# Optimization experiments

Measured on AMD Instinct MI355X. Metric: run time of the kernel, lower is better.

Reference implementation:

```python
import jax, jax.numpy as jnp
import numpy as np

N = 8192
IN_DIM = 256
OUT_DIM = 256


def setup_inputs() -> dict:
    key = jax.random.key(0)
    k1, k2, k3, k4 = jax.random.split(key, 4)
    x = jax.random.normal(k1, (N, IN_DIM), dtype=jnp.float32)
    adj = jax.random.uniform(k2, (N, N), dtype=jnp.float32)
    # nn.Linear(in_dim, out_dim): weight [out,in], bias [out]. Store W as [in,out].
    bound = 1.0 / np.sqrt(IN_DIM)
    W = jax.random.uniform(k3, (IN_DIM, OUT_DIM), dtype=jnp.float32, minval=-bound, maxval=bound)
    b = jax.random.uniform(k4, (OUT_DIM,), dtype=jnp.float32, minval=-bound, maxval=bound)
    return {"x": x, "adj": adj, "W": W, "b": b}


def reference(x, adj, W, b):
    # ReLU( D^{-1/2} (A + I) D^{-1/2} X W + b )
    # A_hat = adj + I; degree = A_hat.sum(axis=1)
    n = adj.shape[0]
    A_hat = adj + jnp.eye(n, dtype=adj.dtype)
    degree = A_hat.sum(axis=1)
    d_inv_sqrt = degree ** -0.5  # [N]
    # D^{-1/2} @ A_hat @ D^{-1/2} == row-scale then col-scale (no NxN diag matmuls)
    A_norm = A_hat * d_inv_sqrt[:, None] * d_inv_sqrt[None, :]
    out = A_norm @ x          # [N, in_dim]
    out = out @ W + b         # [N, out_dim]
    return jax.nn.relu(out)
```

## Files before the change

kernel.cpp:

```cpp
#include <hip/hip_runtime.h>


typedef __attribute__((ext_vector_type(8))) short short8;
typedef __attribute__((ext_vector_type(4))) float floatx4;

#define GLDS16(g, l) __builtin_amdgcn_global_load_lds(\
    (const __attribute__((address_space(1))) void*)(g), \
    (__attribute__((address_space(3))) void*)(l), 16, 0, 0)

__device__ __forceinline__ unsigned short f2b(float f) {
  unsigned int x = __builtin_bit_cast(unsigned int, f);
  unsigned int r = (x + 0x7fffu + ((x >> 16) & 1u)) >> 16;
  return (unsigned short)r;
}

__global__ __launch_bounds__(512) void k_deg(
    const float* __restrict__ adj, unsigned short* __restrict__ adjb,
    float* __restrict__ degree8) {
  __shared__ __align__(16) char xlds[65536];
  const int t = threadIdx.x, g = t >> 5, c = t & 31;
  const int mb2 = blockIdx.x >> 3, sk = (blockIdx.x >> 1) & 3, h = blockIdx.x & 1;
  const float* src = adj + (size_t)mb2 * 128 * 8192 + sk * 2048 + h * 1024;
  unsigned short* dstP = adjb
      + ((size_t)(mb2 * 4 + sk) * 32768 + (size_t)h * 16384) * 8;
  float rs[8] = {};
#pragma unroll
  for (int s = 0; s < 4; ++s) {
#pragma unroll
    for (int rr = 0; rr < 8; ++rr) {
      const int row = rr * 16 + g;
      const float* p = src + (size_t)row * 8192 + s * 256 + c * 8;
      float4 v0 = *(const float4*)(p);
      float4 v1 = *(const float4*)(p + 4);
      rs[rr] += ((v0.x + v0.y) + (v0.z + v0.w)) + ((v1.x + v1.y) + (v1.z + v1.w));
      short8 u;
      u[0] = f2b(v0.x); u[1] = f2b(v0.y); u[2] = f2b(v0.z); u[3] = f2b(v0.w);
      u[4] = f2b(v1.x); u[5] = f2b(v1.y); u[6] = f2b(v1.z); u[7] = f2b(v1.w);
      *(short8*)(xlds + c * 2048 + ((row ^ (c & 7)) * 16)) = u;
    }
    __syncthreads();
    unsigned short* dst = dstP + (size_t)s * 4096 * 8;
#pragma unroll
    for (int j = 0; j < 8; ++j) {
      const int lu = j * 512 + t;
      const int U = lu >> 7, R = lu & 127;
      short8 u = *(const short8*)(xlds + U * 2048 + ((R ^ (U & 7)) * 16));
      *(short8*)(dst + (size_t)lu * 8) = u;
    }
    __syncthreads();
  }
#pragma unroll
  for (int rr = 0; rr < 8; ++rr) {
#pragma unroll
    for (int o = 16; o > 0; o >>= 1) rs[rr] += __shfl_down(rs[rr], o, 32);
  }
  if (c == 0) {
    float* dp = degree8 + (size_t)(sk * 2 + h) * 8192 + mb2 * 128;
#pragma unroll
    for (int rr = 0; rr < 8; ++rr) dp[rr * 16 + g] = rs[rr];
  }
}

__global__ __launch_bounds__(256) void k_xw(
    const float* __restrict__ X, const float* __restrict__ W,
    const float* __restrict__ bias, const float* __restrict__ degree8,
    float* __restrict__ Zd, unsigned short* __restrict__ Zsb,
    float* __restrict__ sinv) {
  __shared__ unsigned short ldsT[256 * 20];
  const int t = threadIdx.x, l = t & 63, w = t >> 6;
  const int m0 = blockIdx.x * 16;
  const int r0 = w * 4;
  const int n0 = l * 4;
  const float* Xp = X + (size_t)(m0 + r0) * 256;
  float acc[4][4] = {};
#pragma unroll 2
  for (int k = 0; k < 256; k += 4) {
    float4 wv[4];
#pragma unroll
    for (int j = 0; j < 4; ++j) wv[j] = *(const float4*)(W + (size_t)(k + j) * 256 + n0);
#pragma unroll
    for (int r = 0; r < 4; ++r) {
      float4 xv = *(const float4*)(Xp + r * 256 + k);
      const float xs[4] = {xv.x, xv.y, xv.z, xv.w};
#pragma unroll
      for (int j = 0; j < 4; ++j) {
        acc[r][0] += xs[j] * wv[j].x;
        acc[r][1] += xs[j] * wv[j].y;
        acc[r][2] += xs[j] * wv[j].z;
        acc[r][3] += xs[j] * wv[j].w;
      }
    }
  }
  const float4 bv = *(const float4*)(bias + n0);
#pragma unroll
  for (int r = 0; r < 4; ++r) {
    const int row = m0 + r0 + r;
    float deg = 0.f;
#pragma unroll
    for (int p = 0; p < 8; ++p) deg += degree8[(size_t)p * 8192 + row];
    const float sr = rsqrtf(deg + 1.0f);
    if (l == 0) sinv[row] = sr;
    float4 zd;
    zd.x = sr * sr * acc[r][0] + bv.x;
    zd.y = sr * sr * acc[r][1] + bv.y;
    zd.z = sr * sr * acc[r][2] + bv.z;
    zd.w = sr * sr * acc[r][3] + bv.w;
    *(float4*)(Zd + (size_t)row * 256 + n0) = zd;
#pragma unroll
    for (int n = 0; n < 4; ++n)
      ldsT[(size_t)(n0 + n) * 20 + (r0 + r)] = f2b(sr * acc[r][n]);
  }
  __syncthreads();
  const int kt = m0 >> 6, kcb = (m0 >> 3) & 7;
#pragma unroll
  for (int c = 0; c < 2; ++c) {
    const unsigned short* p = ldsT + (size_t)t * 20 + c * 8;
    short8 vv;
#pragma unroll
    for (int j = 0; j < 8; ++j) vv[j] = p[j];
    *(short8*)(Zsb + ((size_t)kt * 2048 + (kcb + c) * 256 + t) * 8) = vv;
  }
}

__global__ __launch_bounds__(256, 2) void k_main(
    const unsigned short* __restrict__ adjb, const unsigned short* __restrict__ Zsb,
    float* __restrict__ P) {
  __shared__ __align__(16) char lds[2][33024];
  const int t = threadIdx.x, l = t & 63, w = t >> 6;
  const int quad = l >> 4, nl = l & 15;
  const int bm2 = blockIdx.x >> 3, bn = (blockIdx.x >> 2) & 1, sk = blockIdx.x & 3;
  const int wm = w & 1, wn = w >> 1;
  const unsigned short* aBase = adjb + (size_t)(bm2 * 4 + sk) * 32768 * 8;
  const unsigned short* bBase = Zsb + ((size_t)sk * 32 * 2048 + bn * 128) * 8;
  floatx4 acc[4][4] = {};

#pragma unroll
  for (int p = 0; p < 4; ++p) {
    const int j = p * 256 + t;
    const int q = j >> 7, rr = j & 127;
    GLDS16(aBase + (size_t)j * 8, lds[0] + q * 2064 + rr * 16);
    GLDS16(bBase + (size_t)(q * 256 + rr) * 8, lds[0] + 16512 + q * 2064 + rr * 16);
  }
  __syncthreads();

  for (int i = 0; i < 32; ++i) {
    const int cur = i & 1, nxt = cur ^ 1;
    const int ib = i < 31 ? i + 1 : 31;
#pragma unroll
    for (int p = 0; p < 4; ++p) {
      const int j = p * 256 + t;
      const int q = j >> 7, rr = j & 127;
      GLDS16(aBase + ((size_t)ib * 1024 + j) * 8, lds[nxt] + q * 2064 + rr * 16);
      GLDS16(bBase + ((size_t)ib * 2048 + q * 256 + rr) * 8,
             lds[nxt] + 16512 + q * 2064 + rr * 16);
    }
    const char* rA = lds[cur];
    const char* rB = lds[cur] + 16512;
#pragma unroll
    for (int kk = 0; kk < 2; ++kk) {
      const int qq = kk * 4 + quad;
      short8 af[4], bf[4];
#pragma unroll
      for (int mi = 0; mi < 4; ++mi)
        af[mi] = *(const short8*)(rA + qq * 2064 + (wm * 64 + mi * 16 + nl) * 16);
#pragma unroll
      for (int nf = 0; nf < 4; ++nf)
        bf[nf] = *(const short8*)(rB + qq * 2064 + (wn * 64 + nf * 16 + nl) * 16);
#pragma unroll
      for (int mi = 0; mi < 4; ++mi)
#pragma unroll
        for (int nf = 0; nf < 4; ++nf)
          acc[mi][nf] = __builtin_amdgcn_mfma_f32_16x16x32_bf16(af[mi], bf[nf], acc[mi][nf], 0, 0, 0);
    }
    __syncthreads();
  }

  float* Pk = P + (size_t)sk * 8192 * 256 + (size_t)bn * 128;
#pragma unroll
  for (int mi = 0; mi < 4; ++mi)
#pragma unroll
    for (int nf = 0; nf < 4; ++nf)
#pragma unroll
      for (int r = 0; r < 4; ++r) {
        const int row = bm2 * 128 + wm * 64 + mi * 16 + quad * 4 + r;
        const int col = wn * 64 + nf * 16 + nl;
        Pk[(size_t)row * 256 + col] = acc[mi][nf][r];
      }
}

__global__ __launch_bounds__(256) void k_fin(
    const float* __restrict__ P, const float* __restrict__ Zd,
    const float* __restrict__ sinv, float* __restrict__ out) {
  const int i = blockIdx.x * 256 + threadIdx.x;
  const int row = i >> 6;
  const float sr = sinv[row];
  const size_t stride = (size_t)8192 * 256;
  float4 p0 = *(const float4*)(P + (size_t)i * 4);
  float4 p1 = *(const float4*)(P + stride + (size_t)i * 4);
  float4 p2 = *(const float4*)(P + 2 * stride + (size_t)i * 4);
  float4 p3 = *(const float4*)(P + 3 * stride + (size_t)i * 4);
  const float4 zd = *(const float4*)(Zd + (size_t)i * 4);
  float4 v;
  v.x = sr * ((p0.x + p1.x) + (p2.x + p3.x)) + zd.x;
  v.y = sr * ((p0.y + p1.y) + (p2.y + p3.y)) + zd.y;
  v.z = sr * ((p0.z + p1.z) + (p2.z + p3.z)) + zd.z;
  v.w = sr * ((p0.w + p1.w) + (p2.w + p3.w)) + zd.w;
  v.x = v.x > 0.f ? v.x : 0.f;
  v.y = v.y > 0.f ? v.y : 0.f;
  v.z = v.z > 0.f ? v.z : 0.f;
  v.w = v.w > 0.f ? v.w : 0.f;
  *(float4*)(out + (size_t)i * 4) = v;
}

extern "C" void kernel_launch(void* const* d_in, const int* in_sizes, int n_in,
                              void* d_out, int out_size, void* d_ws, size_t ws_size,
                              hipStream_t stream) {
  const float* X    = (const float*)d_in[0];
  const float* adj  = (const float*)d_in[1];
  const float* W    = (const float*)d_in[2];
  const float* bias = (const float*)d_in[3];
  float* out = (float*)d_out;
  char* ws = (char*)d_ws;

  float* degree8       = (float*)(ws);
  float* sinv          = (float*)(ws + (512 << 10));
  float* Zd            = (float*)(ws + (1 << 20));
  unsigned short* Zsb  = (unsigned short*)(ws + (9 << 20));
  float* P             = (float*)(ws + (13 << 20));
  unsigned short* adjb = (unsigned short*)(ws + (45 << 20));

  hipLaunchKernelGGL(k_deg,  dim3(512),  dim3(512), 0, stream, adj, adjb, degree8);
  hipLaunchKernelGGL(k_xw,   dim3(512),  dim3(256), 0, stream, X, W, bias, degree8, Zd, Zsb, sinv);
  hipLaunchKernelGGL(k_main, dim3(512),  dim3(256), 0, stream, adjb, Zsb, P);
  hipLaunchKernelGGL(k_fin,  dim3(2048), dim3(256), 0, stream, P, Zd, sinv, out);
}
```

Baseline: 525.2 us.

## Triple-buffer k_main LDS pipeline with half-size K stages and raised occupancy

The main bf16 MFMA loop moves from a double-buffered pipeline with 64-wide K tiles to a three-stage ring of 32-wide K tiles. Explicit vmcnt waits and raw barriers replace __syncthreads, so two tiles can be in flight while one is computed. Launch bounds are raised to 3 blocks per CU, since each block now uses less LDS. MFMA sections are also wrapped in s_setprio. The risk is twice as many barriers per K and fragile hand-written wait counts.

```diff
diff --git a/kernel.cpp b/kernel.cpp
--- a/kernel.cpp
+++ b/kernel.cpp
@@ -122,58 +122,73 @@
   }
 }
 
-__global__ __launch_bounds__(256, 2) void k_main(
+#define LDS_STG 16512
+
+#define STAGE_TILE(ib, s) do {                                               \
+    char* bp_ = &lds[0][0] + (s) * LDS_STG;                                  \
+    _Pragma("unroll")                                                        \
+    for (int p_ = 0; p_ < 2; ++p_) {                                         \
+      const int j_ = p_ * 256 + t;                                           \
+      const int q_ = j_ >> 7, rr_ = j_ & 127;                                \
+      GLDS16(aBase + ((size_t)(ib) * 512 + j_) * 8,                          \
+             bp_ + q_ * 2064 + rr_ * 16);                                    \
+      GLDS16(bBase + ((size_t)(ib) * 1024 + q_ * 256 + rr_) * 8,             \
+             bp_ + 8256 + q_ * 2064 + rr_ * 16);                             \
+    }                                                                        \
+  } while (0)
+
+#define K_COMPUTE(s) do {                                                    \
+    const char* rA_ = &lds[0][0] + (s) * LDS_STG;                            \
+    const char* rB_ = rA_ + 8256;                                            \
+    short8 af_[4], bf_[4];                                                   \
+    _Pragma("unroll")                                                        \
+    for (int mi_ = 0; mi_ < 4; ++mi_)                                        \
+      af_[mi_] = *(const short8*)(rA_ + quad * 2064 + (wm * 64 + mi_ * 16 + nl) * 16); \
+    _Pragma("unroll")                                                        \
+    for (int nf_ = 0; nf_ < 4; ++nf_)                                        \
+      bf_[nf_] = *(const short8*)(rB_ + quad * 2064 + (wn * 64 + nf_ * 16 + nl) * 16); \
+    __builtin_amdgcn_s_setprio(1);                                           \
+    _Pragma("unroll")                                                        \
+    for (int mi_ = 0; mi_ < 4; ++mi_)                                        \
+      _Pragma("unroll")                                                      \
+      for (int nf_ = 0; nf_ < 4; ++nf_)                                      \
+        acc[mi_][nf_] = __builtin_amdgcn_mfma_f32_16x16x32_bf16(             \
+            af_[mi_], bf_[nf_], acc[mi_][nf_], 0, 0, 0);                     \
+    __builtin_amdgcn_s_setprio(0);                                           \
+  } while (0)
+
+#define VMW4 asm volatile("s_waitcnt vmcnt(4)" ::: "memory")
+#define VMW0 asm volatile("s_waitcnt vmcnt(0)" ::: "memory")
+#define RBAR do { __builtin_amdgcn_s_barrier();                              \
+                  __builtin_amdgcn_sched_barrier(0); } while (0)
+
+__global__ __launch_bounds__(256, 3) void k_main(
     const unsigned short* __restrict__ adjb, const unsigned short* __restrict__ Zsb,
     float* __restrict__ P) {
-  __shared__ __align__(16) char lds[2][33024];
+  __shared__ __align__(16) char lds[3][LDS_STG];
   const int t = threadIdx.x, l = t & 63, w = t >> 6;
   const int quad = l >> 4, nl = l & 15;
   const int bm2 = blockIdx.x >> 3, bn = (blockIdx.x >> 2) & 1, sk = blockIdx.x & 3;
   const int wm = w & 1, wn = w >> 1;
   const unsigned short* aBase = adjb + (size_t)(bm2 * 4 + sk) * 32768 * 8;
-  const unsigned short* bBase = Zsb + ((size_t)sk * 32 * 2048 + bn * 128) * 8;
+  const unsigned short* bBase = Zsb + ((size_t)sk * 65536 + bn * 128) * 8;
   floatx4 acc[4][4] = {};
 
-#pragma unroll
-  for (int p = 0; p < 4; ++p) {
-    const int j = p * 256 + t;
-    const int q = j >> 7, rr = j & 127;
-    GLDS16(aBase + (size_t)j * 8, lds[0] + q * 2064 + rr * 16);
-    GLDS16(bBase + (size_t)(q * 256 + rr) * 8, lds[0] + 16512 + q * 2064 + rr * 16);
-  }
-  __syncthreads();
-
-  for (int i = 0; i < 32; ++i) {
-    const int cur = i & 1, nxt = cur ^ 1;
-    const int ib = i < 31 ? i + 1 : 31;
-#pragma unroll
-    for (int p = 0; p < 4; ++p) {
-      const int j = p * 256 + t;
-      const int q = j >> 7, rr = j & 127;
-      GLDS16(aBase + ((size_t)ib * 1024 + j) * 8, lds[nxt] + q * 2064 + rr * 16);
-      GLDS16(bBase + ((size_t)ib * 2048 + q * 256 + rr) * 8,
-             lds[nxt] + 16512 + q * 2064 + rr * 16);
-    }
-    const char* rA = lds[cur];
-    const char* rB = lds[cur] + 16512;
-#pragma unroll
-    for (int kk = 0; kk < 2; ++kk) {
-      const int qq = kk * 4 + quad;
-      short8 af[4], bf[4];
-#pragma unroll
-      for (int mi = 0; mi < 4; ++mi)
-        af[mi] = *(const short8*)(rA + qq * 2064 + (wm * 64 + mi * 16 + nl) * 16);
-#pragma unroll
-      for (int nf = 0; nf < 4; ++nf)
-        bf[nf] = *(const short8*)(rB + qq * 2064 + (wn * 64 + nf * 16 + nl) * 16);
-#pragma unroll
-      for (int mi = 0; mi < 4; ++mi)
-#pragma unroll
-        for (int nf = 0; nf < 4; ++nf)
-          acc[mi][nf] = __builtin_amdgcn_mfma_f32_16x16x32_bf16(af[mi], bf[nf], acc[mi][nf], 0, 0, 0);
-    }
-    __syncthreads();
-  }
+  STAGE_TILE(0, 0);
+  STAGE_TILE(1, 1);
+
+  int cur = 0;
+  for (int i = 0; i < 62; ++i) {
+    VMW4;
+    RBAR;
+    const int nb = cur + 2 >= 3 ? cur - 1 : cur + 2;
+    STAGE_TILE(i + 2, nb);
+    K_COMPUTE(cur);
+    cur = cur + 1 == 3 ? 0 : cur + 1;
+  }
+  VMW4; RBAR; K_COMPUTE(cur);
+  cur = cur + 1 == 3 ? 0 : cur + 1;
+  VMW0; RBAR; K_COMPUTE(cur);
 
   float* Pk = P + (size_t)sk * 8192 * 256 + (size_t)bn * 128;
 #pragma unroll
```

Measured after the change: 524.8 us. Within noise of the previous version (-0.1%).
